# Kernel tuning notes

Hardware: AMD Instinct MI355X
Metric: run time of the kernel (lower is better)

Reference implementation:

```python
import jax, jax.numpy as jnp
import numpy as np

B, S, H = 1, 2048, 2048
NH, NKV, HD = 32, 8, 64
GROUPS = NH // NKV
KV_DIM = NKV * HD
COMP = int(S * 0.5)
FF = 5632  # round_up(2048*4*2/3, 256), fla GatedMLP convention
DEPTH = 2
EPS = 1e-6


def rmsnorm(x, w):
    var = jnp.mean(jnp.square(x), axis=-1, keepdims=True)
    return x * jax.lax.rsqrt(var + EPS) * w


def setup_inputs() -> dict:
    key = jax.random.key(0)
    ks = jax.random.split(key, 10)
    sc = 0.02
    return {
        "hidden_states": jax.random.normal(ks[0], (B, S, H), jnp.float32),
        "comp_w": jax.random.normal(ks[1], (COMP, S), jnp.float32) * sc,
        "comp_b": jnp.zeros((COMP,), jnp.float32),
        "q_w": jax.random.normal(ks[2], (H, H), jnp.float32) * sc,
        "k_w": jax.random.normal(ks[3], (KV_DIM, H), jnp.float32) * sc,
        "v_w": jax.random.normal(ks[4], (KV_DIM, H), jnp.float32) * sc,
        "o_w": jax.random.normal(ks[5], (H, H), jnp.float32) * sc,
        "attn_norm_w": jnp.ones((H,), jnp.float32),
        "mlp_norm_w": jnp.ones((H,), jnp.float32),
        "gate_w": jax.random.normal(ks[6], (FF, H), jnp.float32) * sc,
        "up_w": jax.random.normal(ks[7], (FF, H), jnp.float32) * sc,
        "down_w": jax.random.normal(ks[8], (H, FF), jnp.float32) * sc,
    }


def reference(hidden_states, comp_w, comp_b, q_w, k_w, v_w, o_w,
              attn_norm_w, mlp_norm_w, gate_w, up_w, down_w):
    # init_compressed_tokens: Linear over the sequence axis
    # (b,s,h) -> transpose -> (b,h,s) @ W^T -> (b,h,c) -> transpose -> (b,c,h)
    compressed = jnp.einsum('bsh,cs->bch', hidden_states, comp_w) + comp_b[None, :, None]

    for _ in range(DEPTH):
        residual = jnp.concatenate([hidden_states, compressed], axis=1)  # (b, s+c, h)
        ct = rmsnorm(compressed, attn_norm_w)
        q = (ct @ q_w.T).reshape(B, COMP, NH, HD)
        k = (residual @ k_w.T).reshape(B, S + COMP, NKV, HD)
        v = (residual @ v_w.T).reshape(B, S + COMP, NKV, HD)
        # GQA expand (repeat_interleave along head dim)
        k = jnp.repeat(k, GROUPS, axis=2)
        v = jnp.repeat(v, GROUPS, axis=2)
        scores = jnp.einsum('bsnk,btnk->bsnt', q, k) / (HD ** 0.5)
        attn = jax.nn.softmax(scores, axis=-1)
        o = jnp.einsum('bsnt,btnk->bsnk', attn, v).reshape(B, COMP, H)
        compressed = o @ o_w.T + ct
        ct2 = rmsnorm(compressed, mlp_norm_w)
        mlp_out = (jax.nn.silu(ct2 @ gate_w.T) * (ct2 @ up_w.T)) @ down_w.T
        compressed = mlp_out + ct2
    return compressed
```

## Files before the change

kernel.cpp:

```cpp
#include <hip/hip_runtime.h>
#include <math.h>

constexpr int S_   = 2048;
constexpr int H_   = 2048;
constexpr int NH_  = 32;
constexpr int NKV_ = 8;
constexpr int HD_  = 64;
constexpr int GROUPS_ = NH_ / NKV_;
constexpr int KV_  = NKV_ * HD_;
constexpr int KV2_ = 2 * KV_;
constexpr int COMP_ = 1024;
constexpr int FF_  = 5632;
constexpr int GU2_ = 2 * FF_;
constexpr int TOT_ = S_ + COMP_;
constexpr float EPS_ = 1e-6f;
constexpr int SK_ = 4;
constexpr int SP_ = 2;
constexpr float LOG2E_ = 1.44269504088896340736f;

typedef __attribute__((ext_vector_type(4))) float f32x4;
typedef __attribute__((ext_vector_type(8))) short bf16x8;
typedef __attribute__((ext_vector_type(8))) ushort u16x8;

__device__ __forceinline__ ushort f2bf(float x) {
    union { float f; unsigned u; } v; v.f = x;
    unsigned r = v.u + 0x7fffu + ((v.u >> 16) & 1u);
    return (ushort)(r >> 16);
}
__device__ __forceinline__ float bf2f(ushort x) {
    union { unsigned u; float f; } v; v.u = ((unsigned)x) << 16;
    return v.f;
}

__global__ __launch_bounds__(256) void f2b_k(
    const float* __restrict__ x, ushort* __restrict__ y, int n4)
{
    int i = blockIdx.x * 256 + threadIdx.x;
    const int stride = gridDim.x * 256;
    for (; i < n4; i += stride) {
        float4 v = ((const float4*)x)[i];
        ushort4 r = {f2bf(v.x), f2bf(v.y), f2bf(v.z), f2bf(v.w)};
        ((ushort4*)y)[i] = r;
    }
}

__global__ __launch_bounds__(256) void tpose64(
    const ushort* __restrict__ in, ushort* __restrict__ out,
    int R, int C, int ldi)
{
    __shared__ ushort T[64][72];
    const int r0 = blockIdx.x * 64, c0 = blockIdx.y * 64;
    const int row = threadIdx.x >> 2, seg = threadIdx.x & 3;

    const ushort* g = &in[(size_t)(r0 + row) * ldi + c0 + seg * 16];
    *(u16x8*)&T[row][seg * 16]     = *(const u16x8*)g;
    *(u16x8*)&T[row][seg * 16 + 8] = *(const u16x8*)(g + 8);
    __syncthreads();

    ushort tmp[16];
#pragma unroll
    for (int j = 0; j < 16; j++) tmp[j] = T[seg * 16 + j][row];
    ushort* go = &out[(size_t)(c0 + row) * R + r0 + seg * 16];
    *(u16x8*)go       = *(const u16x8*)&tmp[0];
    *(u16x8*)(go + 8) = *(const u16x8*)&tmp[8];
}

__global__ __launch_bounds__(256) void mfma_gemm(
    const ushort* __restrict__ A, const ushort* __restrict__ B,
    const float* __restrict__ addp, const float* __restrict__ bias,
    float oscale, float* __restrict__ outf, ushort* __restrict__ outb,
    int M, int N, int K)
{
    __shared__ ushort Alds[128 * 32];
    __shared__ ushort Blds[128 * 32];

    const int tid  = threadIdx.x;
    const int w    = tid >> 6;
    const int lane = tid & 63;
    const int bm = blockIdx.y, bn = blockIdx.x;
    const int wr = w >> 1, wc = w & 1;
    const int fr = lane & 15;
    const int fq = lane >> 4;
    const int srow = lane >> 2;
    const int skof = (lane & 3) * 8;

    f32x4 acc[4][4];
#pragma unroll
    for (int i = 0; i < 4; i++)
#pragma unroll
        for (int j = 0; j < 4; j++)
            acc[i][j] = (f32x4){0.f, 0.f, 0.f, 0.f};

    for (int k0 = 0; k0 < K; k0 += 32) {
        __syncthreads();
#pragma unroll
        for (int i = 0; i < 2; i++) {
            const int slot = w * 2 + i;
            const ushort* ga = &A[(size_t)(bm * 128 + slot * 16 + srow) * K + k0 + skof];
            __builtin_amdgcn_global_load_lds(
                (const __attribute__((address_space(1))) void*)ga,
                (__attribute__((address_space(3))) void*)&Alds[slot * 512], 16, 0, 0);
            const ushort* gb = &B[(size_t)(bn * 128 + slot * 16 + srow) * K + k0 + skof];
            __builtin_amdgcn_global_load_lds(
                (const __attribute__((address_space(1))) void*)gb,
                (__attribute__((address_space(3))) void*)&Blds[slot * 512], 16, 0, 0);
        }
        __syncthreads();

        bf16x8 a[4], b[4];
#pragma unroll
        for (int mt = 0; mt < 4; mt++)
            a[mt] = *(const bf16x8*)&Alds[(wr * 64 + mt * 16 + fr) * 32 + fq * 8];
#pragma unroll
        for (int nt = 0; nt < 4; nt++)
            b[nt] = *(const bf16x8*)&Blds[(wc * 64 + nt * 16 + fr) * 32 + fq * 8];

#pragma unroll
        for (int mt = 0; mt < 4; mt++)
#pragma unroll
            for (int nt = 0; nt < 4; nt++)
                acc[mt][nt] = __builtin_amdgcn_mfma_f32_16x16x32_bf16(
                    a[mt], b[nt], acc[mt][nt], 0, 0, 0);
    }

#pragma unroll
    for (int mt = 0; mt < 4; mt++) {
#pragma unroll
        for (int nt = 0; nt < 4; nt++) {
#pragma unroll
            for (int r = 0; r < 4; r++) {
                const int row = bm * 128 + wr * 64 + mt * 16 + fq * 4 + r;
                const int col = bn * 128 + wc * 64 + nt * 16 + fr;
                float v = acc[mt][nt][r] * oscale;
                if (bias) v += bias[row];
                if (addp) v += addp[(size_t)row * N + col];
                if (outf) outf[(size_t)row * N + col] = v;
                if (outb) outb[(size_t)row * N + col] = f2bf(v);
            }
        }
    }
}

#define BARS do { __builtin_amdgcn_s_barrier(); __builtin_amdgcn_sched_barrier(0); } while (0)
#define VMW(n) asm volatile("s_waitcnt vmcnt(" #n ")" ::: "memory")
#define STG(gp, lp) __builtin_amdgcn_global_load_lds( \
    (const __attribute__((address_space(1))) void*)(gp), \
    (__attribute__((address_space(3))) void*)(lp), 16, 0, 0)
#define STA(bufA, R0, kt) STG(Ag + (size_t)(R0) * K + (kt) * 64, &(bufA)[((R0) + w * 8) * 64])
#define STB(bufB, R0, kt) STG(Bg + (size_t)(R0) * K + (kt) * 64, &(bufB)[((R0) + w * 8) * 64])

__device__ __forceinline__ void ldaq(bf16x8 (&aa)[2][2], const ushort* bufA,
                                     int m0, int aoff, int s0, int s1)
{
#pragma unroll
    for (int m = 0; m < 2; m++) {
        aa[m][0] = *(const bf16x8*)&bufA[aoff + (m0 + m) * 1024 + s0];
        aa[m][1] = *(const bf16x8*)&bufA[aoff + (m0 + m) * 1024 + s1];
    }
}
__device__ __forceinline__ void ldbq(bf16x8 (&bb)[4][2], const ushort* bufB,
                                     int boff, int s0, int s1)
{
#pragma unroll
    for (int nt = 0; nt < 4; nt++) {
        bb[nt][0] = *(const bf16x8*)&bufB[boff + nt * 1024 + s0];
        bb[nt][1] = *(const bf16x8*)&bufB[boff + nt * 1024 + s1];
    }
}
template <int M0>
__device__ __forceinline__ void mfmaq(f32x4 (&acc)[8][4], bf16x8 (&aa)[2][2],
                                      bf16x8 (&bb)[4][2])
{
    __builtin_amdgcn_s_setprio(1);
#pragma unroll
    for (int m = 0; m < 2; m++)
#pragma unroll
        for (int nt = 0; nt < 4; nt++) {
            acc[M0 + m][nt] = __builtin_amdgcn_mfma_f32_16x16x32_bf16(
                aa[m][0], bb[nt][0], acc[M0 + m][nt], 0, 0, 0);
            acc[M0 + m][nt] = __builtin_amdgcn_mfma_f32_16x16x32_bf16(
                aa[m][1], bb[nt][1], acc[M0 + m][nt], 0, 0, 0);
        }
    __builtin_amdgcn_s_setprio(0);
}

__global__ __launch_bounds__(512, 2) void gemm8ph(
    const ushort* __restrict__ A, const ushort* __restrict__ B,
    ushort* __restrict__ C, int N, int K)
{
    alignas(16) __shared__ ushort lds[4][16384];
    ushort* const lA0 = lds[0];
    ushort* const lB0 = lds[1];
    ushort* const lA1 = lds[2];
    ushort* const lB1 = lds[3];

    const int tid = threadIdx.x;
    const int w = tid >> 6, lane = tid & 63;
    const int wr = w >> 2, wc = w & 3;
    const int fr = lane & 15, fq = lane >> 4;
    const int xk = fr & 7;

    const int nwg = gridDim.x;
    const int nbn = N >> 8;
    int id = (int)blockIdx.x;
    if (!(nwg & 7)) id = (id & 7) * (nwg >> 3) + (id >> 3);
    const int bm = id / nbn, bn = id - bm * nbn;

    const int srow = lane >> 3;
    const int scol = ((lane & 7) ^ srow) << 3;
    const ushort* Ag = A + (size_t)(bm * 256 + w * 8 + srow) * K + scol;
    const ushort* Bg = B + (size_t)(bn * 256 + w * 8 + srow) * K + scol;

    const int aoff = (wr * 128 + fr) * 64;
    const int boff = (wc * 64 + fr) * 64;
    const int s0 = ((0 + fq) ^ xk) << 3;
    const int s1 = ((4 + fq) ^ xk) << 3;

    f32x4 acc[8][4];
#pragma unroll
    for (int i = 0; i < 8; i++)
#pragma unroll
        for (int j = 0; j < 4; j++) acc[i][j] = (f32x4){0.f, 0.f, 0.f, 0.f};

    bf16x8 aa[2][2], bb[4][2];

    STB(lB0, 0, 0);   STB(lB0, 64, 0);
    STA(lA0, 0, 0);   STA(lA0, 128, 0);
    STB(lB0, 128, 0); STB(lB0, 192, 0);
    STA(lA0, 64, 0);  STA(lA0, 192, 0);
    STB(lB1, 0, 1);   STB(lB1, 64, 1);
    STA(lA1, 0, 1);   STA(lA1, 128, 1);
    STB(lB1, 128, 1); STB(lB1, 192, 1);
    VMW(6);
    BARS;

    const int NITER = K >> 7;
    for (int i = 0; i < NITER - 1; i++) {
        const int t1 = 2 * i + 1, t2 = 2 * i + 2, t3 = 2 * i + 3;
        ldbq(bb, lB0, boff, s0, s1);
        ldaq(aa, lA0, 0, aoff, s0, s1);
        STA(lA1, 64, t1); STA(lA1, 192, t1);
        BARS; mfmaq<0>(acc, aa, bb); BARS;
        ldaq(aa, lA0, 2, aoff, s0, s1);
        STB(lB0, 0, t2); STB(lB0, 64, t2);
        BARS; mfmaq<2>(acc, aa, bb); BARS;
        ldaq(aa, lA0, 4, aoff, s0, s1);
        STA(lA0, 0, t2); STA(lA0, 128, t2);
        BARS; mfmaq<4>(acc, aa, bb); BARS;
        ldaq(aa, lA0, 6, aoff, s0, s1);
        STB(lB0, 128, t2); STB(lB0, 192, t2);
        BARS; mfmaq<6>(acc, aa, bb); VMW(6); BARS;
        ldbq(bb, lB1, boff, s0, s1);
        ldaq(aa, lA1, 0, aoff, s0, s1);
        STA(lA0, 64, t2); STA(lA0, 192, t2);
        BARS; mfmaq<0>(acc, aa, bb); BARS;
        ldaq(aa, lA1, 2, aoff, s0, s1);
        STB(lB1, 0, t3); STB(lB1, 64, t3);
        BARS; mfmaq<2>(acc, aa, bb); BARS;
        ldaq(aa, lA1, 4, aoff, s0, s1);
        STA(lA1, 0, t3); STA(lA1, 128, t3);
        BARS; mfmaq<4>(acc, aa, bb); BARS;
        ldaq(aa, lA1, 6, aoff, s0, s1);
        STB(lB1, 128, t3); STB(lB1, 192, t3);
        BARS; mfmaq<6>(acc, aa, bb); VMW(6); BARS;
    }
    {
        const int t1 = 2 * NITER - 1;
        ldbq(bb, lB0, boff, s0, s1);
        ldaq(aa, lA0, 0, aoff, s0, s1);
        STA(lA1, 64, t1); STA(lA1, 192, t1);
        BARS; mfmaq<0>(acc, aa, bb); BARS;
        ldaq(aa, lA0, 2, aoff, s0, s1);
        BARS; mfmaq<2>(acc, aa, bb); BARS;
        ldaq(aa, lA0, 4, aoff, s0, s1);
        BARS; mfmaq<4>(acc, aa, bb); BARS;
        ldaq(aa, lA0, 6, aoff, s0, s1);
        BARS; mfmaq<6>(acc, aa, bb); VMW(0); BARS;
        ldbq(bb, lB1, boff, s0, s1);
        ldaq(aa, lA1, 0, aoff, s0, s1);
        BARS; mfmaq<0>(acc, aa, bb); BARS;
        ldaq(aa, lA1, 2, aoff, s0, s1);
        BARS; mfmaq<2>(acc, aa, bb); BARS;
        ldaq(aa, lA1, 4, aoff, s0, s1);
        BARS; mfmaq<4>(acc, aa, bb); BARS;
        ldaq(aa, lA1, 6, aoff, s0, s1);
        mfmaq<6>(acc, aa, bb);
    }

    ushort* Cb = C + (size_t)(bm * 256 + wr * 128 + fq * 4) * N
                   + bn * 256 + wc * 64 + fr;
#pragma unroll
    for (int mt = 0; mt < 8; mt++)
#pragma unroll
        for (int nt = 0; nt < 4; nt++)
#pragma unroll
            for (int r = 0; r < 4; r++)
                Cb[(size_t)(mt * 16 + r) * N + nt * 16] = f2bf(acc[mt][nt][r]);
}

__global__ __launch_bounds__(256) void mfma_gemm_sk(
    const ushort* __restrict__ A, const ushort* __restrict__ B,
    float* __restrict__ part, int M, int N, int K, int Kc)
{
    __shared__ ushort Alds[128 * 32];
    __shared__ ushort Blds[128 * 32];

    const int tid  = threadIdx.x;
    const int w    = tid >> 6;
    const int lane = tid & 63;
    const int bm = blockIdx.y, bn = blockIdx.x, z = blockIdx.z;
    const int wr = w >> 1, wc = w & 1;
    const int fr = lane & 15;
    const int fq = lane >> 4;
    const int srow = lane >> 2;
    const int skof = (lane & 3) * 8;

    f32x4 acc[4][4];
#pragma unroll
    for (int i = 0; i < 4; i++)
#pragma unroll
        for (int j = 0; j < 4; j++)
            acc[i][j] = (f32x4){0.f, 0.f, 0.f, 0.f};

    const int kbeg = z * Kc;
    for (int k0 = kbeg; k0 < kbeg + Kc; k0 += 32) {
        __syncthreads();
#pragma unroll
        for (int i = 0; i < 2; i++) {
            const int slot = w * 2 + i;
            const ushort* ga = &A[(size_t)(bm * 128 + slot * 16 + srow) * K + k0 + skof];
            __builtin_amdgcn_global_load_lds(
                (const __attribute__((address_space(1))) void*)ga,
                (__attribute__((address_space(3))) void*)&Alds[slot * 512], 16, 0, 0);
            const ushort* gb = &B[(size_t)(bn * 128 + slot * 16 + srow) * K + k0 + skof];
            __builtin_amdgcn_global_load_lds(
                (const __attribute__((address_space(1))) void*)gb,
                (__attribute__((address_space(3))) void*)&Blds[slot * 512], 16, 0, 0);
        }
        __syncthreads();

        bf16x8 a[4], b[4];
#pragma unroll
        for (int mt = 0; mt < 4; mt++)
            a[mt] = *(const bf16x8*)&Alds[(wr * 64 + mt * 16 + fr) * 32 + fq * 8];
#pragma unroll
        for (int nt = 0; nt < 4; nt++)
            b[nt] = *(const bf16x8*)&Blds[(wc * 64 + nt * 16 + fr) * 32 + fq * 8];

#pragma unroll
        for (int mt = 0; mt < 4; mt++)
#pragma unroll
            for (int nt = 0; nt < 4; nt++)
                acc[mt][nt] = __builtin_amdgcn_mfma_f32_16x16x32_bf16(
                    a[mt], b[nt], acc[mt][nt], 0, 0, 0);
    }

    float* pz = part + (size_t)z * M * N;
#pragma unroll
    for (int mt = 0; mt < 4; mt++)
#pragma unroll
        for (int nt = 0; nt < 4; nt++)
#pragma unroll
            for (int r = 0; r < 4; r++) {
                const int row = bm * 128 + wr * 64 + mt * 16 + fq * 4 + r;
                const int col = bn * 128 + wc * 64 + nt * 16 + fr;
                pz[(size_t)row * N + col] = acc[mt][nt][r];
            }
}

__global__ __launch_bounds__(256) void sk_reduce(
    const float* __restrict__ part, int mn4, int n4,
    const float* __restrict__ bias, const float* __restrict__ addp,
    float oscale, float* __restrict__ outf, ushort* __restrict__ outb)
{
    const size_t mn = (size_t)mn4 * 4;
    int i = blockIdx.x * 256 + threadIdx.x;
    const int stride = gridDim.x * 256;
    for (; i < mn4; i += stride) {
        float4 v = ((const float4*)part)[i];
#pragma unroll
        for (int z = 1; z < SK_; z++) {
            const float4 pz = ((const float4*)(part + z * mn))[i];
            v.x += pz.x; v.y += pz.y; v.z += pz.z; v.w += pz.w;
        }
        v.x *= oscale; v.y *= oscale; v.z *= oscale; v.w *= oscale;
        if (bias) {
            const float bb = bias[i / n4];
            v.x += bb; v.y += bb; v.z += bb; v.w += bb;
        }
        if (addp) {
            const float4 ad = ((const float4*)addp)[i];
            v.x += ad.x; v.y += ad.y; v.z += ad.z; v.w += ad.w;
        }
        if (outf) ((float4*)outf)[i] = v;
        if (outb) {
            ushort4 r = {f2bf(v.x), f2bf(v.y), f2bf(v.z), f2bf(v.w)};
            ((ushort4*)outb)[i] = r;
        }
    }
}

__global__ __launch_bounds__(256) void attn_mfma(
    const ushort* __restrict__ q, const ushort* __restrict__ k, int ldk,
    const ushort* __restrict__ vt, float* __restrict__ attp,
    float* __restrict__ ml)
{
    constexpr int LDT = 72;
    constexpr int KSPAN = TOT_ / SP_;
    __shared__ ushort Ks[64 * LDT];
    __shared__ ushort Vs[64 * LDT];
    __shared__ ushort Ps[64 * LDT];

    const int qt = blockIdx.x, h = blockIdx.y, z = blockIdx.z;
    const int kvh = h / GROUPS_;
    const int tid = threadIdx.x;
    const int w = tid >> 6, lane = tid & 63;
    const int fr = lane & 15, fq = lane >> 4;
    const int q0 = qt * 64;

    const ushort* qrow = &q[(size_t)(q0 + w * 16 + fr) * H_ + h * HD_];
    const bf16x8 bq0 = *(const bf16x8*)(qrow + fq * 8);
    const bf16x8 bq1 = *(const bf16x8*)(qrow + 32 + fq * 8);

    float m = -1e30f, l = 0.f;
    f32x4 acc[4];
#pragma unroll
    for (int nt = 0; nt < 4; nt++) acc[nt] = (f32x4){0.f, 0.f, 0.f, 0.f};

    const int t_beg = z * KSPAN;
    for (int t0 = t_beg; t0 < t_beg + KSPAN; t0 += 64) {
        __syncthreads();
        {
            const int row = tid >> 2, seg = tid & 3;
            const ushort* gk = &k[(size_t)(t0 + row) * ldk + kvh * HD_ + seg * 16];
            u16x8 k0v = *(const u16x8*)gk;
            u16x8 k1v = *(const u16x8*)(gk + 8);
            const ushort* gv = &vt[(size_t)(kvh * HD_ + row) * TOT_ + t0 + seg * 16];
            u16x8 v0v = *(const u16x8*)gv;
            u16x8 v1v = *(const u16x8*)(gv + 8);
            *(u16x8*)&Ks[row * LDT + seg * 16]     = k0v;
            *(u16x8*)&Ks[row * LDT + seg * 16 + 8] = k1v;
            *(u16x8*)&Vs[row * LDT + seg * 16]     = v0v;
            *(u16x8*)&Vs[row * LDT + seg * 16 + 8] = v1v;
        }
        __syncthreads();

        f32x4 st[4];
#pragma unroll
        for (int nt = 0; nt < 4; nt++) {
            bf16x8 a0 = *(const bf16x8*)&Ks[(nt * 16 + fr) * LDT + fq * 8];
            bf16x8 a1 = *(const bf16x8*)&Ks[(nt * 16 + fr) * LDT + 32 + fq * 8];
            f32x4 t = (f32x4){0.f, 0.f, 0.f, 0.f};
            t = __builtin_amdgcn_mfma_f32_16x16x32_bf16(a0, bq0, t, 0, 0, 0);
            t = __builtin_amdgcn_mfma_f32_16x16x32_bf16(a1, bq1, t, 0, 0, 0);
            st[nt] = t;
        }

        float mt = st[0][0];
#pragma unroll
        for (int nt = 0; nt < 4; nt++)
#pragma unroll
            for (int r = 0; r < 4; r++) mt = fmaxf(mt, st[nt][r]);
        mt = fmaxf(mt, __shfl_xor(mt, 16));
        mt = fmaxf(mt, __shfl_xor(mt, 32));
        const float mn = fmaxf(m, mt);
        const float alpha = exp2f(m - mn);
        m = mn;
        float ss = 0.f;
#pragma unroll
        for (int nt = 0; nt < 4; nt++)
#pragma unroll
            for (int r = 0; r < 4; r++) {
                const float pv = exp2f(st[nt][r] - mn);
                st[nt][r] = pv;
                ss += pv;
            }
        ss += __shfl_xor(ss, 16);
        ss += __shfl_xor(ss, 32);
        l = l * alpha + ss;

#pragma unroll
        for (int nt = 0; nt < 4; nt++) {
            ushort4 pk = {f2bf(st[nt][0]), f2bf(st[nt][1]),
                          f2bf(st[nt][2]), f2bf(st[nt][3])};
            *(ushort4*)&Ps[(w * 16 + fr) * LDT + nt * 16 + fq * 4] = pk;
        }

        bf16x8 ap0 = *(const bf16x8*)&Ps[(w * 16 + fr) * LDT + fq * 8];
        bf16x8 ap1 = *(const bf16x8*)&Ps[(w * 16 + fr) * LDT + 32 + fq * 8];
        float ar[4];
#pragma unroll
        for (int r = 0; r < 4; r++) ar[r] = __shfl(alpha, fq * 4 + r, 16);
#pragma unroll
        for (int nt = 0; nt < 4; nt++) {
            bf16x8 b0 = *(const bf16x8*)&Vs[(nt * 16 + fr) * LDT + fq * 8];
            bf16x8 b1 = *(const bf16x8*)&Vs[(nt * 16 + fr) * LDT + 32 + fq * 8];
            f32x4 t = acc[nt];
            t[0] *= ar[0]; t[1] *= ar[1]; t[2] *= ar[2]; t[3] *= ar[3];
            t = __builtin_amdgcn_mfma_f32_16x16x32_bf16(ap0, b0, t, 0, 0, 0);
            t = __builtin_amdgcn_mfma_f32_16x16x32_bf16(ap1, b1, t, 0, 0, 0);
            acc[nt] = t;
        }
    }

    float* pz = attp + (size_t)z * COMP_ * H_;
#pragma unroll
    for (int r = 0; r < 4; r++) {
        const int row = q0 + w * 16 + fq * 4 + r;
#pragma unroll
        for (int nt = 0; nt < 4; nt++)
            pz[(size_t)row * H_ + h * HD_ + nt * 16 + fr] = acc[nt][r];
    }
    if (lane < 16)
        ((float2*)ml)[((size_t)z * NH_ + h) * COMP_ + (q0 + w * 16 + fr)] =
            make_float2(m, l);
}

__global__ __launch_bounds__(256) void attn_merge(
    const float* __restrict__ attp, const float* __restrict__ ml,
    ushort* __restrict__ o, int n4)
{
    constexpr int H4 = H_ / 4;
    constexpr size_t PS = (size_t)COMP_ * H_;
    int i = blockIdx.x * 256 + threadIdx.x;
    const int stride = gridDim.x * 256;
    for (; i < n4; i += stride) {
        const int row = i / H4;
        const int col = (i - row * H4) * 4;
        const int h = col >> 6;
        const float2 ml0 = ((const float2*)ml)[((size_t)0 * NH_ + h) * COMP_ + row];
        const float2 ml1 = ((const float2*)ml)[((size_t)1 * NH_ + h) * COMP_ + row];
        const float M = fmaxf(ml0.x, ml1.x);
        const float a0 = exp2f(ml0.x - M), a1 = exp2f(ml1.x - M);
        const float inv = 1.0f / (a0 * ml0.y + a1 * ml1.y);
        const float4 p0 = ((const float4*)attp)[i];
        const float4 p1 = ((const float4*)(attp + PS))[i];
        ushort4 r = {f2bf((a0 * p0.x + a1 * p1.x) * inv),
                     f2bf((a0 * p0.y + a1 * p1.y) * inv),
                     f2bf((a0 * p0.z + a1 * p1.z) * inv),
                     f2bf((a0 * p0.w + a1 * p1.w) * inv)};
        ((ushort4*)o)[i] = r;
    }
}

__global__ __launch_bounds__(256) void rmsnorm_dual_k(
    const float* __restrict__ x, const float* __restrict__ w,
    float* __restrict__ y, ushort* __restrict__ yb)
{
    const int row = blockIdx.x;
    const float* xr = x + (size_t)row * H_;
    __shared__ float red[256];

    float s = 0.f;
#pragma unroll
    for (int i = 0; i < 8; i++) {
        const float v = xr[threadIdx.x + i * 256];
        s += v * v;
    }
    red[threadIdx.x] = s;
    __syncthreads();
    for (int t = 128; t > 0; t >>= 1) {
        if (threadIdx.x < t) red[threadIdx.x] += red[threadIdx.x + t];
        __syncthreads();
    }
    const float scale = rsqrtf(red[0] * (1.0f / H_) + EPS_);
#pragma unroll
    for (int i = 0; i < 8; i++) {
        const int idx = threadIdx.x + i * 256;
        const float v = xr[idx] * scale * w[idx];
        y[(size_t)row * H_ + idx] = v;
        yb[(size_t)row * H_ + idx] = f2bf(v);
    }
}

__global__ __launch_bounds__(256) void silu_mul_gu(
    const ushort* __restrict__ gu, ushort* __restrict__ g, int n4)
{
    constexpr int FF4 = FF_ / 4;
    int i = blockIdx.x * 256 + threadIdx.x;
    const int stride = gridDim.x * 256;
    for (; i < n4; i += stride) {
        const int row = i / FF4;
        const int c = (i - row * FF4) * 4;
        ushort4 gv = *(const ushort4*)&gu[(size_t)row * GU2_ + c];
        ushort4 uv = *(const ushort4*)&gu[(size_t)row * GU2_ + FF_ + c];
        float x0 = bf2f(gv.x), x1 = bf2f(gv.y), x2 = bf2f(gv.z), x3 = bf2f(gv.w);
        x0 = x0 / (1.f + __expf(-x0)) * bf2f(uv.x);
        x1 = x1 / (1.f + __expf(-x1)) * bf2f(uv.y);
        x2 = x2 / (1.f + __expf(-x2)) * bf2f(uv.z);
        x3 = x3 / (1.f + __expf(-x3)) * bf2f(uv.w);
        ushort4 r = {f2bf(x0), f2bf(x1), f2bf(x2), f2bf(x3)};
        ((ushort4*)g)[i] = r;
    }
}

extern "C" void kernel_launch(void* const* d_in, const int* in_sizes, int n_in,
                              void* d_out, int out_size, void* d_ws, size_t ws_size,
                              hipStream_t stream)
{
    (void)in_sizes; (void)n_in; (void)out_size; (void)ws_size;

    const float* hidden      = (const float*)d_in[0];
    const float* comp_w      = (const float*)d_in[1];
    const float* comp_b      = (const float*)d_in[2];
    const float* q_w         = (const float*)d_in[3];
    const float* k_w         = (const float*)d_in[4];
    const float* v_w         = (const float*)d_in[5];
    const float* o_w         = (const float*)d_in[6];
    const float* attn_norm_w = (const float*)d_in[7];
    const float* mlp_norm_w  = (const float*)d_in[8];
    const float* gate_w      = (const float*)d_in[9];
    const float* up_w        = (const float*)d_in[10];
    const float* down_w      = (const float*)d_in[11];
    float* out = (float*)d_out;

    char* p = (char*)d_ws;
    auto alloc = [&](size_t bytes) -> char* {
        char* r = p; p += (bytes + 255) & ~(size_t)255; return r;
    };
    ushort* qw_bf    = (ushort*)alloc((size_t)H_ * H_ * 2);
    ushort* kvw_bf   = (ushort*)alloc((size_t)KV2_ * H_ * 2);
    ushort* ow_bf    = (ushort*)alloc((size_t)H_ * H_ * 2);
    ushort* guw_bf   = (ushort*)alloc((size_t)GU2_ * H_ * 2);
    ushort* down_bf  = (ushort*)alloc((size_t)H_ * FF_ * 2);
    ushort* compw_bf = (ushort*)alloc((size_t)COMP_ * S_ * 2);
    ushort* hidcomp  = (ushort*)alloc((size_t)TOT_ * H_ * 2);
    ushort* hidT     = (ushort*)alloc((size_t)H_ * S_ * 2);
    ushort* ct_bf    = (ushort*)alloc((size_t)COMP_ * H_ * 2);
    ushort* ct2_bf   = (ushort*)alloc((size_t)COMP_ * H_ * 2);
    ushort* ob_bf    = (ushort*)alloc((size_t)COMP_ * H_ * 2);
    ushort* qb_bf    = (ushort*)alloc((size_t)COMP_ * H_ * 2);
    ushort* kvb_bf   = (ushort*)alloc((size_t)TOT_ * KV2_ * 2);
    ushort* vt_bf    = (ushort*)alloc((size_t)KV_ * TOT_ * 2);
    ushort* gb_bf    = (ushort*)alloc((size_t)COMP_ * FF_ * 2);
    float* comp0 = (float*)alloc((size_t)COMP_ * H_ * 4);
    float* comp1 = (float*)alloc((size_t)COMP_ * H_ * 4);
    float* ct    = (float*)alloc((size_t)COMP_ * H_ * 4);
    float* ct2   = (float*)alloc((size_t)COMP_ * H_ * 4);
    float*  skbuf = (float*)alloc((size_t)SK_ * TOT_ * KV2_ * 4);
    ushort* gub   = (ushort*)skbuf;
    float*  attp  = skbuf;
    float*  mlbuf = skbuf + (size_t)SP_ * COMP_ * H_;

    ushort* cur_bf = hidcomp + (size_t)S_ * H_;

    const dim3 blk(256);

    f2b_k<<<512, blk, 0, stream>>>(q_w,    qw_bf,            H_ * H_ / 4);
    f2b_k<<<512, blk, 0, stream>>>(k_w,    kvw_bf,           KV_ * H_ / 4);
    f2b_k<<<512, blk, 0, stream>>>(v_w,    kvw_bf + (size_t)KV_ * H_, KV_ * H_ / 4);
    f2b_k<<<512, blk, 0, stream>>>(o_w,    ow_bf,            H_ * H_ / 4);
    f2b_k<<<512, blk, 0, stream>>>(gate_w, guw_bf,           FF_ * H_ / 4);
    f2b_k<<<512, blk, 0, stream>>>(up_w,   guw_bf + (size_t)FF_ * H_, FF_ * H_ / 4);
    f2b_k<<<512, blk, 0, stream>>>(down_w, down_bf,          H_ * FF_ / 4);
    f2b_k<<<512, blk, 0, stream>>>(comp_w, compw_bf,         COMP_ * S_ / 4);
    f2b_k<<<512, blk, 0, stream>>>(hidden, hidcomp,          S_ * H_ / 4);
    tpose64<<<dim3(S_ / 64, H_ / 64), blk, 0, stream>>>(hidcomp, hidT, S_, H_, H_);

    mfma_gemm_sk<<<dim3(H_ / 128, COMP_ / 128, SK_), blk, 0, stream>>>(
        compw_bf, hidT, skbuf, COMP_, H_, S_, S_ / SK_);
    sk_reduce<<<1024, blk, 0, stream>>>(
        skbuf, COMP_ * H_ / 4, H_ / 4, comp_b, nullptr, 1.f, comp0, cur_bf);

    float* cur = comp0;
    for (int d = 0; d < 2; d++) {
        rmsnorm_dual_k<<<COMP_, blk, 0, stream>>>(cur, attn_norm_w, ct, ct_bf);

        mfma_gemm_sk<<<dim3(H_ / 128, COMP_ / 128, SK_), blk, 0, stream>>>(
            ct_bf, qw_bf, skbuf, COMP_, H_, H_, H_ / SK_);
        sk_reduce<<<1024, blk, 0, stream>>>(
            skbuf, COMP_ * H_ / 4, H_ / 4, nullptr, nullptr, 0.125f * LOG2E_,
            nullptr, qb_bf);

        mfma_gemm_sk<<<dim3(KV2_ / 128, TOT_ / 128, SK_), blk, 0, stream>>>(
            hidcomp, kvw_bf, skbuf, TOT_, KV2_, H_, H_ / SK_);
        sk_reduce<<<1024, blk, 0, stream>>>(
            skbuf, TOT_ * KV2_ / 4, KV2_ / 4, nullptr, nullptr, 1.f, nullptr, kvb_bf);

        tpose64<<<dim3(TOT_ / 64, KV_ / 64), blk, 0, stream>>>(
            kvb_bf + KV_, vt_bf, TOT_, KV_, KV2_);

        attn_mfma<<<dim3(COMP_ / 64, NH_, SP_), blk, 0, stream>>>(
            qb_bf, kvb_bf, KV2_, vt_bf, attp, mlbuf);
        attn_merge<<<512, blk, 0, stream>>>(attp, mlbuf, ob_bf, COMP_ * H_ / 4);

        mfma_gemm_sk<<<dim3(H_ / 128, COMP_ / 128, SK_), blk, 0, stream>>>(
            ob_bf, ow_bf, skbuf, COMP_, H_, H_, H_ / SK_);
        sk_reduce<<<1024, blk, 0, stream>>>(
            skbuf, COMP_ * H_ / 4, H_ / 4, nullptr, ct, 1.f, comp1, nullptr);

        rmsnorm_dual_k<<<COMP_, blk, 0, stream>>>(comp1, mlp_norm_w, ct2, ct2_bf);

        gemm8ph<<<dim3((GU2_ / 256) * (COMP_ / 256)), dim3(512), 0, stream>>>(
            ct2_bf, guw_bf, gub, GU2_, H_);

        silu_mul_gu<<<1024, blk, 0, stream>>>(gub, gb_bf, COMP_ * FF_ / 4);

        float* dst = (d == 1) ? out : comp0;
        ushort* dst_bf = (d == 1) ? nullptr : cur_bf;
        mfma_gemm_sk<<<dim3(H_ / 128, COMP_ / 128, SK_), blk, 0, stream>>>(
            gb_bf, down_bf, skbuf, COMP_, H_, FF_, FF_ / SK_);
        sk_reduce<<<1024, blk, 0, stream>>>(
            skbuf, COMP_ * H_ / 4, H_ / 4, nullptr, ct2, 1.f, dst, dst_bf);
        cur = dst;
    }
}
```

Baseline: 914.2 us.

## Double-buffer attention K/V tiles via direct global-to-LDS loads with lazy rescale

Rewrites the attention inner loop to prefetch the next K/V tile straight into LDS with global_load_lds into a double buffer, so the load overlaps the current tile's MFMAs and one barrier per iteration is dropped. The LDS layout is now MFMA-fragment order, which removes the padded rows. The online softmax skips rescaling the running max and accumulator unless the max rises by more than 8 (log2 units), and P is packed with v_cvt_pk_bf16 into an XOR-swizzled buffer. s_setprio hints are added around the MFMA blocks. The costs are double the K/V LDS footprint, and the lazy rescale lets the exponentials grow up to 2^8, which may slightly change rounding.

```diff
diff --git a/kernel.cpp b/kernel.cpp
--- a/kernel.cpp
+++ b/kernel.cpp
@@ -30,6 +30,11 @@
 __device__ __forceinline__ float bf2f(ushort x) {
     union { unsigned u; float f; } v; v.u = ((unsigned)x) << 16;
     return v.f;
+}
+__device__ __forceinline__ uint cvtpk_bf16(float lo, float hi) {
+    uint r;
+    asm("v_cvt_pk_bf16_f32 %0, %1, %2" : "=v"(r) : "v"(lo), "v"(hi));
+    return r;
 }
 
 __global__ __launch_bounds__(256) void f2b_k(
@@ -405,11 +410,10 @@
     const ushort* __restrict__ vt, float* __restrict__ attp,
     float* __restrict__ ml)
 {
-    constexpr int LDT = 72;
     constexpr int KSPAN = TOT_ / SP_;
-    __shared__ ushort Ks[64 * LDT];
-    __shared__ ushort Vs[64 * LDT];
-    __shared__ ushort Ps[64 * LDT];
+    alignas(16) __shared__ ushort Kb[2][8 * 512];
+    alignas(16) __shared__ ushort Vb[2][8 * 512];
+    alignas(16) __shared__ ushort Ps[64 * 64];
 
     const int qt = blockIdx.x, h = blockIdx.y, z = blockIdx.z;
     const int kvh = h / GROUPS_;
@@ -428,32 +432,48 @@
     for (int nt = 0; nt < 4; nt++) acc[nt] = (f32x4){0.f, 0.f, 0.f, 0.f};
 
     const int t_beg = z * KSPAN;
-    for (int t0 = t_beg; t0 < t_beg + KSPAN; t0 += 64) {
-        __syncthreads();
-        {
-            const int row = tid >> 2, seg = tid & 3;
-            const ushort* gk = &k[(size_t)(t0 + row) * ldk + kvh * HD_ + seg * 16];
-            u16x8 k0v = *(const u16x8*)gk;
-            u16x8 k1v = *(const u16x8*)(gk + 8);
-            const ushort* gv = &vt[(size_t)(kvh * HD_ + row) * TOT_ + t0 + seg * 16];
-            u16x8 v0v = *(const u16x8*)gv;
-            u16x8 v1v = *(const u16x8*)(gv + 8);
-            *(u16x8*)&Ks[row * LDT + seg * 16]     = k0v;
-            *(u16x8*)&Ks[row * LDT + seg * 16 + 8] = k1v;
-            *(u16x8*)&Vs[row * LDT + seg * 16]     = v0v;
-            *(u16x8*)&Vs[row * LDT + seg * 16 + 8] = v1v;
-        }
-        __syncthreads();
-
+    const ushort* kp = &k[(size_t)(t_beg + w * 16 + fr) * ldk + kvh * HD_ + fq * 8];
+    const ushort* vp = &vt[(size_t)(kvh * HD_ + w * 16 + fr) * TOT_ + t_beg + fq * 8];
+
+#define ASTG(gp, lp) __builtin_amdgcn_global_load_lds( \
+    (const __attribute__((address_space(1))) void*)(gp), \
+    (__attribute__((address_space(3))) void*)(lp), 16, 0, 0)
+
+    ASTG(kp,      &Kb[0][w * 512]);
+    ASTG(kp + 32, &Kb[0][(4 + w) * 512]);
+    ASTG(vp,      &Vb[0][w * 512]);
+    ASTG(vp + 32, &Vb[0][(4 + w) * 512]);
+    asm volatile("s_waitcnt vmcnt(0)" ::: "memory");
+    __syncthreads();
+    const ushort* kn = kp + (size_t)64 * ldk;
+    const ushort* vn = vp + 64;
+
+    const int pxor = (fr & 7) << 4;
+    char* const psb = (char*)&Ps[(w * 16 + fr) * 64];
+
+    const int NT = KSPAN / 64;
+    int cur = 0;
+    for (int t = 0; t < NT; t++) {
         f32x4 st[4];
+        __builtin_amdgcn_s_setprio(1);
 #pragma unroll
         for (int nt = 0; nt < 4; nt++) {
-            bf16x8 a0 = *(const bf16x8*)&Ks[(nt * 16 + fr) * LDT + fq * 8];
-            bf16x8 a1 = *(const bf16x8*)&Ks[(nt * 16 + fr) * LDT + 32 + fq * 8];
-            f32x4 t = (f32x4){0.f, 0.f, 0.f, 0.f};
-            t = __builtin_amdgcn_mfma_f32_16x16x32_bf16(a0, bq0, t, 0, 0, 0);
-            t = __builtin_amdgcn_mfma_f32_16x16x32_bf16(a1, bq1, t, 0, 0, 0);
-            st[nt] = t;
+            const bf16x8 a0 = *(const bf16x8*)&Kb[cur][(nt * 64 + lane) * 8];
+            const bf16x8 a1 = *(const bf16x8*)&Kb[cur][((4 + nt) * 64 + lane) * 8];
+            f32x4 tacc = (f32x4){0.f, 0.f, 0.f, 0.f};
+            tacc = __builtin_amdgcn_mfma_f32_16x16x32_bf16(a0, bq0, tacc, 0, 0, 0);
+            tacc = __builtin_amdgcn_mfma_f32_16x16x32_bf16(a1, bq1, tacc, 0, 0, 0);
+            st[nt] = tacc;
+        }
+        __builtin_amdgcn_s_setprio(0);
+
+        if (t + 1 < NT) {
+            ASTG(kn,      &Kb[cur ^ 1][w * 512]);
+            ASTG(kn + 32, &Kb[cur ^ 1][(4 + w) * 512]);
+            ASTG(vn,      &Vb[cur ^ 1][w * 512]);
+            ASTG(vn + 32, &Vb[cur ^ 1][(4 + w) * 512]);
+            kn += (size_t)64 * ldk;
+            vn += 64;
         }
 
         float mt = st[0][0];
@@ -463,45 +483,59 @@
             for (int r = 0; r < 4; r++) mt = fmaxf(mt, st[nt][r]);
         mt = fmaxf(mt, __shfl_xor(mt, 16));
         mt = fmaxf(mt, __shfl_xor(mt, 32));
-        const float mn = fmaxf(m, mt);
-        const float alpha = exp2f(m - mn);
-        m = mn;
+        if (!__all(mt <= m + 8.0f)) {
+            const float mnew = fmaxf(m, mt);
+            const float alpha = exp2f(m - mnew);
+            m = mnew;
+            l *= alpha;
+            const float ar0 = __shfl(alpha, fq * 4 + 0, 16);
+            const float ar1 = __shfl(alpha, fq * 4 + 1, 16);
+            const float ar2 = __shfl(alpha, fq * 4 + 2, 16);
+            const float ar3 = __shfl(alpha, fq * 4 + 3, 16);
+#pragma unroll
+            for (int nt = 0; nt < 4; nt++) {
+                acc[nt][0] *= ar0; acc[nt][1] *= ar1;
+                acc[nt][2] *= ar2; acc[nt][3] *= ar3;
+            }
+        }
         float ss = 0.f;
 #pragma unroll
         for (int nt = 0; nt < 4; nt++)
 #pragma unroll
             for (int r = 0; r < 4; r++) {
-                const float pv = exp2f(st[nt][r] - mn);
+                const float pv = exp2f(st[nt][r] - m);
                 st[nt][r] = pv;
                 ss += pv;
             }
         ss += __shfl_xor(ss, 16);
         ss += __shfl_xor(ss, 32);
-        l = l * alpha + ss;
+        l += ss;
 
 #pragma unroll
         for (int nt = 0; nt < 4; nt++) {
-            ushort4 pk = {f2bf(st[nt][0]), f2bf(st[nt][1]),
-                          f2bf(st[nt][2]), f2bf(st[nt][3])};
-            *(ushort4*)&Ps[(w * 16 + fr) * LDT + nt * 16 + fq * 4] = pk;
-        }
-
-        bf16x8 ap0 = *(const bf16x8*)&Ps[(w * 16 + fr) * LDT + fq * 8];
-        bf16x8 ap1 = *(const bf16x8*)&Ps[(w * 16 + fr) * LDT + 32 + fq * 8];
-        float ar[4];
-#pragma unroll
-        for (int r = 0; r < 4; r++) ar[r] = __shfl(alpha, fq * 4 + r, 16);
+            uint2 uu;
+            uu.x = cvtpk_bf16(st[nt][0], st[nt][1]);
+            uu.y = cvtpk_bf16(st[nt][2], st[nt][3]);
+            *(uint2*)(psb + ((nt * 32 + fq * 8) ^ pxor)) = uu;
+        }
+        const bf16x8 ap0 = *(const bf16x8*)(psb + ((fq * 16) ^ pxor));
+        const bf16x8 ap1 = *(const bf16x8*)(psb + ((64 + fq * 16) ^ pxor));
+
+        __builtin_amdgcn_s_setprio(1);
 #pragma unroll
         for (int nt = 0; nt < 4; nt++) {
-            bf16x8 b0 = *(const bf16x8*)&Vs[(nt * 16 + fr) * LDT + fq * 8];
-            bf16x8 b1 = *(const bf16x8*)&Vs[(nt * 16 + fr) * LDT + 32 + fq * 8];
-            f32x4 t = acc[nt];
-            t[0] *= ar[0]; t[1] *= ar[1]; t[2] *= ar[2]; t[3] *= ar[3];
-            t = __builtin_amdgcn_mfma_f32_16x16x32_bf16(ap0, b0, t, 0, 0, 0);
-            t = __builtin_amdgcn_mfma_f32_16x16x32_bf16(ap1, b1, t, 0, 0, 0);
-            acc[nt] = t;
-        }
-    }
+            const bf16x8 b0 = *(const bf16x8*)&Vb[cur][(nt * 64 + lane) * 8];
+            const bf16x8 b1 = *(const bf16x8*)&Vb[cur][((4 + nt) * 64 + lane) * 8];
+            acc[nt] = __builtin_amdgcn_mfma_f32_16x16x32_bf16(ap0, b0, acc[nt], 0, 0, 0);
+            acc[nt] = __builtin_amdgcn_mfma_f32_16x16x32_bf16(ap1, b1, acc[nt], 0, 0, 0);
+        }
+        __builtin_amdgcn_s_setprio(0);
+
+        asm volatile("s_waitcnt vmcnt(0)" ::: "memory");
+        __syncthreads();
+        cur ^= 1;
+    }
+#undef ASTG
 
     float* pz = attp + (size_t)z * COMP_ * H_;
 #pragma unroll
```

Result: faster. 887.6 us (-2.9%).
